# Kernel optimization log

Measured on AMD Instinct MI355X. Metric: run time of the kernel, lower is better.

## Reference

```python
import jax, jax.numpy as jnp
import numpy as np

N, E, IN_DIM, C = 30000, 300000, 128, 16


def _xavier(key, shape):
    fan_in, fan_out = shape[1], shape[0]
    lim = np.sqrt(6.0 / (fan_in + fan_out))
    return jax.random.uniform(key, shape, jnp.float32, -lim, lim)


def layernorm(x, g, b, eps=1e-5):
    mu = jnp.mean(x, axis=-1, keepdims=True)
    var = jnp.var(x, axis=-1, keepdims=True)
    return (x - mu) * jax.lax.rsqrt(var + eps) * g + b


def setup_inputs() -> dict:
    key = jax.random.key(0)
    ks = jax.random.split(key, 8)
    D9 = C * 9            # 144
    DI = C * (C * 2)      # 512
    return {
        "x": jax.random.normal(ks[0], (N, IN_DIM), jnp.float32),
        "h": jax.random.normal(ks[1], (N, IN_DIM), jnp.float32),
        "local_frames": jax.random.normal(ks[2], (N, 3, 3), jnp.float32),
        "edge_index": jax.random.randint(ks[3], (2, E), 0, N, jnp.int64),
        "batch": jnp.zeros((N,), jnp.int64),
        # tensor_init: Linear(IN_DIM,144) LN SiLU Linear(144,144) LN SiLU
        "W1": _xavier(ks[4], (D9, IN_DIM)), "b1": jnp.zeros((D9,), jnp.float32),
        "g1": jnp.ones((D9,), jnp.float32), "be1": jnp.zeros((D9,), jnp.float32),
        "W2": _xavier(ks[5], (D9, D9)), "b2": jnp.zeros((D9,), jnp.float32),
        "g2": jnp.ones((D9,), jnp.float32), "be2": jnp.zeros((D9,), jnp.float32),
        # tensor_interaction: Linear(2*IN_DIM,512) LN Sigmoid
        "Wi": _xavier(ks[6], (DI, 2 * IN_DIM)), "bi": jnp.zeros((DI,), jnp.float32),
        "gi": jnp.ones((DI,), jnp.float32), "bei": jnp.zeros((DI,), jnp.float32),
    }


def reference(x, h, local_frames, edge_index, batch,
              W1, b1, g1, be1, W2, b2, g2, be2, Wi, bi, gi, bei):
    n = x.shape[0]
    row, col = edge_index[0], edge_index[1]

    # tensor_init(h) -> [N, C, 3, 3]
    t = jax.nn.silu(layernorm(h @ W1.T + b1, g1, be1))
    t = jax.nn.silu(layernorm(t @ W2.T + b2, g2, be2))
    tensors = t.reshape(n, C, 3, 3)

    hi, hj = h[col], h[row]
    ti, tj = tensors[col], tensors[row]
    Ri, Rj = local_frames[col], local_frames[row]

    # R_rel = Ri^T @ Rj : [E,3,3]
    R_rel = jnp.einsum('eki,ekj->eij', Ri, Rj)
    # rotate sender tensor: R_rel T R_rel^T
    tj_in_i = jnp.einsum('eik,eckl,elj->ecij', R_rel, tj, R_rel)

    stacked_tensor = jnp.concatenate([ti, tj_in_i], axis=1)          # [E,2C,3,3]
    stacked_scalars = jnp.concatenate([hi, hj], axis=-1)             # [E,2*IN_DIM]
    w = jax.nn.sigmoid(layernorm(stacked_scalars @ Wi.T + bi, gi, bei))
    int_weights = w.reshape(-1, 2 * C, C)                            # [E,2C,C]

    t_new = jnp.einsum('ekij,ekc->ecij', stacked_tensor, int_weights)  # [E,C,3,3]

    t_out = jax.ops.segment_sum(t_new, col, num_segments=n)           # [N,C,3,3]
    t_out = 0.5 * (t_out + jnp.swapaxes(t_out, -1, -2))
    return t_out
```

## Files before the change

kernel.cpp:

```cpp
#include <hip/hip_runtime.h>

#define NN 30000
#define EE 300000
#define HD 128
#define D9 144
#define ECHUNK 150000

typedef unsigned int uint32;
typedef unsigned short u16;
typedef __attribute__((ext_vector_type(8))) short short8;
typedef __attribute__((ext_vector_type(4))) float f32x4;
typedef __attribute__((ext_vector_type(4))) uint32 u32x4;

__device__ __forceinline__ float sigmoidf_(float x){ return 1.0f/(1.0f+__expf(-x)); }
__device__ __forceinline__ float siluf_(float x){ return x/(1.0f+__expf(-x)); }
__device__ __forceinline__ u16 f2bf(float f){
  uint32 u = __float_as_uint(f);
  return (u16)((u + 0x7fffu + ((u>>16)&1u)) >> 16);
}
__device__ __forceinline__ float bf2f(u16 b){ return __uint_as_float(((uint32)b)<<16); }
__device__ __forceinline__ float bflo(uint32 u){ return __uint_as_float(u<<16); }
__device__ __forceinline__ float bfhi(uint32 u){ return __uint_as_float(u & 0xffff0000u); }
__device__ __forceinline__ uint32 pk2(float a, float b){ return (uint32)f2bf(a) | ((uint32)f2bf(b)<<16); }

__global__ __launch_bounds__(256) void cvt_wq_k(const float* __restrict__ Wi, u16* __restrict__ Wq){
  int i = blockIdx.x*256 + threadIdx.x;
  if (i < 512*128){
    int n = i >> 7, k = i & 127;
    float xl = Wi[n*256 + k];
    float xr = Wi[n*256 + 128 + k];
    u16 lh = f2bf(xl);
    Wq[i]          = lh;
    Wq[65536 + i]  = f2bf(xl - bf2f(lh));
    u16 rh = f2bf(xr);
    Wq[131072 + i] = rh;
    Wq[196608 + i] = f2bf(xr - bf2f(rh));
  }
}

__global__ __launch_bounds__(256) void cvt_w1s_k(const float* __restrict__ W1, u16* __restrict__ W1s){
  int i = blockIdx.x*256 + threadIdx.x;
  if (i < 144*128){
    float x = W1[i];
    u16 hh = f2bf(x);
    W1s[i] = hh;
    W1s[18432 + i] = f2bf(x - bf2f(hh));
  }
}
__global__ __launch_bounds__(256) void cvt_w2s_k(const float* __restrict__ W2, u16* __restrict__ W2s){
  int i = blockIdx.x*256 + threadIdx.x;
  if (i < 144*160){
    int r = i / 160, k = i - r*160;
    float x = (k < 144) ? W2[r*144 + k] : 0.f;
    u16 hh = f2bf(x);
    W2s[i] = hh;
    W2s[23040 + i] = f2bf(x - bf2f(hh));
  }
}
__global__ __launch_bounds__(256) void cvt_gt_k(const float* __restrict__ gi, const float* __restrict__ bei,
                                                float* __restrict__ gt, float* __restrict__ bet){
  int i = blockIdx.x*256 + threadIdx.x;
  if (i < 512){
    int c = i & 15, k = i >> 4;
    gt [c*32 + k] = gi[i];
    bet[c*32 + k] = bei[i];
  }
}

__global__ __launch_bounds__(256) void hist_k(const int* __restrict__ ei, uint32* __restrict__ start){
  int e = blockIdx.x*256 + threadIdx.x;
  if (e < EE){
    int col = ei[EE + e];
    col = col < 0 ? 0 : (col >= NN ? NN-1 : col);
    atomicAdd(&start[col], 1u);
  }
}

__global__ __launch_bounds__(1024) void scan_k(uint32* __restrict__ start){
  __shared__ uint32 part[1024];
  const int t = threadIdx.x;
  const int base = t * 30;
  uint32 loc[30];
  uint32 s = 0;
  #pragma unroll
  for (int i = 0; i < 30; ++i){
    int idx = base + i;
    uint32 cv = (idx < NN) ? start[idx] : 0u;
    loc[i] = s;
    s += cv;
  }
  part[t] = s;
  __syncthreads();
  for (int off = 1; off < 1024; off <<= 1){
    uint32 add = (t >= off) ? part[t - off] : 0u;
    __syncthreads();
    part[t] += add;
    __syncthreads();
  }
  uint32 pre = (t == 0) ? 0u : part[t - 1];
  #pragma unroll
  for (int i = 0; i < 30; ++i){
    int idx = base + i;
    if (idx < NN) start[idx] = pre + loc[i];
  }
}

__global__ __launch_bounds__(256) void scatter_k(const int* __restrict__ ei,
                                                 uint32* __restrict__ start,
                                                 u16* __restrict__ srow, u16* __restrict__ scol){
  int e = blockIdx.x*256 + threadIdx.x;
  if (e < EE){
    int row = ei[e];
    row = row < 0 ? 0 : (row >= NN ? NN-1 : row);
    int col = ei[EE + e];
    col = col < 0 ? 0 : (col >= NN ? NN-1 : col);
    uint32 pos = atomicAdd(&start[col], 1u);
    srow[pos] = (u16)row;
    scol[pos] = (u16)col;
  }
}

__global__ __launch_bounds__(256) void tensor_init2_k(
    const float* __restrict__ h,
    const u16* __restrict__ W1s, const u16* __restrict__ W2s,
    const float* __restrict__ b1, const float* __restrict__ g1, const float* __restrict__ be1,
    const float* __restrict__ b2, const float* __restrict__ g2, const float* __restrict__ be2,
    float* __restrict__ tens_t)
{
  __shared__ float t1s[16 * 164];
  __shared__ float pool[160];

  const int t = threadIdx.x;
  const int w = t >> 6, l = t & 63, lr = l & 15, lg = l >> 4;
  const int nb = blockIdx.x * 16;
  const int ntile = (w == 0) ? 3 : 2;
  int tiles[3]; tiles[0] = 2*w; tiles[1] = 2*w + 1; tiles[2] = 8;

  f32x4 acc[3];
  #pragma unroll
  for (int ti = 0; ti < 3; ++ti) acc[ti] = (f32x4){0,0,0,0};
  {
    const float* qA = h + (size_t)(nb + lr) * HD + lg*8;
    #pragma unroll
    for (int ks = 0; ks < 4; ++ks){
      float4 x0 = *(const float4*)(qA + ks*32);
      float4 x1 = *(const float4*)(qA + ks*32 + 4);
      float xs[8] = {x0.x, x0.y, x0.z, x0.w, x1.x, x1.y, x1.z, x1.w};
      short8 aH, aL;
      #pragma unroll
      for (int j = 0; j < 8; ++j){
        u16 hh = f2bf(xs[j]);
        aH[j] = (short)hh;
        aL[j] = (short)f2bf(xs[j] - bf2f(hh));
      }
      for (int ti = 0; ti < ntile; ++ti){
        const u16* b = W1s + (tiles[ti]*16 + lr)*128 + lg*8 + ks*32;
        short8 bH = *(const short8*)b;
        short8 bL = *(const short8*)(b + 18432);
        acc[ti] = __builtin_amdgcn_mfma_f32_16x16x32_bf16(aH, bH, acc[ti], 0, 0, 0);
        acc[ti] = __builtin_amdgcn_mfma_f32_16x16x32_bf16(aL, bH, acc[ti], 0, 0, 0);
        acc[ti] = __builtin_amdgcn_mfma_f32_16x16x32_bf16(aH, bL, acc[ti], 0, 0, 0);
      }
    }
  }
  for (int ti = 0; ti < ntile; ++ti){
    float bb = b1[tiles[ti]*16 + lr];
    #pragma unroll
    for (int r = 0; r < 4; ++r) acc[ti][r] += bb;
  }
  {
    float ps[4], pq[4];
    #pragma unroll
    for (int r = 0; r < 4; ++r){
      float s = 0.f, q = 0.f;
      for (int ti = 0; ti < ntile; ++ti){ s += acc[ti][r]; q += acc[ti][r]*acc[ti][r]; }
      ps[r] = s; pq[r] = q;
    }
    #pragma unroll
    for (int off = 1; off < 16; off <<= 1)
      #pragma unroll
      for (int r = 0; r < 4; ++r){ ps[r] += __shfl_xor(ps[r], off); pq[r] += __shfl_xor(pq[r], off); }
    if (lr == 0){
      #pragma unroll
      for (int r = 0; r < 4; ++r){
        pool[w*32 + (lg*4 + r)*2 + 0] = ps[r];
        pool[w*32 + (lg*4 + r)*2 + 1] = pq[r];
      }
    }
  }
  __syncthreads();
  if (t < 16){
    float s = pool[t*2] + pool[32 + t*2] + pool[64 + t*2] + pool[96 + t*2];
    float q = pool[t*2+1] + pool[32 + t*2+1] + pool[64 + t*2+1] + pool[96 + t*2+1];
    float mu = s * (1.0f/144.0f);
    pool[128 + t] = mu;
    pool[144 + t] = rsqrtf(q * (1.0f/144.0f) - mu*mu + 1e-5f);
  }
  __syncthreads();
  for (int ti = 0; ti < ntile; ++ti){
    int col = tiles[ti]*16 + lr;
    float gg = g1[col], bb = be1[col];
    #pragma unroll
    for (int r = 0; r < 4; ++r){
      int node = lg*4 + r;
      float mu = pool[128 + node], rs = pool[144 + node];
      t1s[node*164 + col] = siluf_((acc[ti][r] - mu) * rs * gg + bb);
    }
  }
  t1s[(t >> 4)*164 + 144 + (t & 15)] = 0.f;
  __syncthreads();

  #pragma unroll
  for (int ti = 0; ti < 3; ++ti) acc[ti] = (f32x4){0,0,0,0};
  #pragma unroll
  for (int ks = 0; ks < 5; ++ks){
    float4 x0 = *(const float4*)&t1s[lr*164 + lg*8 + ks*32];
    float4 x1 = *(const float4*)&t1s[lr*164 + lg*8 + ks*32 + 4];
    float xs[8] = {x0.x, x0.y, x0.z, x0.w, x1.x, x1.y, x1.z, x1.w};
    short8 aH, aL;
    #pragma unroll
    for (int j = 0; j < 8; ++j){
      u16 hh = f2bf(xs[j]);
      aH[j] = (short)hh;
      aL[j] = (short)f2bf(xs[j] - bf2f(hh));
    }
    for (int ti = 0; ti < ntile; ++ti){
      const u16* b = W2s + (tiles[ti]*16 + lr)*160 + lg*8 + ks*32;
      short8 bH = *(const short8*)b;
      short8 bL = *(const short8*)(b + 23040);
      acc[ti] = __builtin_amdgcn_mfma_f32_16x16x32_bf16(aH, bH, acc[ti], 0, 0, 0);
      acc[ti] = __builtin_amdgcn_mfma_f32_16x16x32_bf16(aL, bH, acc[ti], 0, 0, 0);
      acc[ti] = __builtin_amdgcn_mfma_f32_16x16x32_bf16(aH, bL, acc[ti], 0, 0, 0);
    }
  }
  for (int ti = 0; ti < ntile; ++ti){
    float bb = b2[tiles[ti]*16 + lr];
    #pragma unroll
    for (int r = 0; r < 4; ++r) acc[ti][r] += bb;
  }
  __syncthreads();
  {
    float ps[4], pq[4];
    #pragma unroll
    for (int r = 0; r < 4; ++r){
      float s = 0.f, q = 0.f;
      for (int ti = 0; ti < ntile; ++ti){ s += acc[ti][r]; q += acc[ti][r]*acc[ti][r]; }
      ps[r] = s; pq[r] = q;
    }
    #pragma unroll
    for (int off = 1; off < 16; off <<= 1)
      #pragma unroll
      for (int r = 0; r < 4; ++r){ ps[r] += __shfl_xor(ps[r], off); pq[r] += __shfl_xor(pq[r], off); }
    if (lr == 0){
      #pragma unroll
      for (int r = 0; r < 4; ++r){
        pool[w*32 + (lg*4 + r)*2 + 0] = ps[r];
        pool[w*32 + (lg*4 + r)*2 + 1] = pq[r];
      }
    }
  }
  __syncthreads();
  if (t < 16){
    float s = pool[t*2] + pool[32 + t*2] + pool[64 + t*2] + pool[96 + t*2];
    float q = pool[t*2+1] + pool[32 + t*2+1] + pool[64 + t*2+1] + pool[96 + t*2+1];
    float mu = s * (1.0f/144.0f);
    pool[128 + t] = mu;
    pool[144 + t] = rsqrtf(q * (1.0f/144.0f) - mu*mu + 1e-5f);
  }
  __syncthreads();
  for (int ti = 0; ti < ntile; ++ti){
    int col = tiles[ti]*16 + lr;
    float gg = g2[col], bb = be2[col];
    int c = col / 9, m = col - c*9;
    #pragma unroll
    for (int r = 0; r < 4; ++r){
      int node = lg*4 + r;
      float mu = pool[128 + node], rs = pool[144 + node];
      float val = siluf_((acc[ti][r] - mu) * rs * gg + bb);
      tens_t[(size_t)(nb + node)*144 + m*16 + c] = val;
    }
  }
}

__global__ __launch_bounds__(256) void node_gemm_k(
    const float* __restrict__ h, const u16* __restrict__ Wq,
    const float* __restrict__ bi,
    u16* __restrict__ uu_t, u16* __restrict__ v16_t)
{
  const int t = threadIdx.x;
  const int w = t >> 6, l = t & 63, lr = l & 15, lg = l >> 4;
  const int nb = blockIdx.x * 16;

  const float* qA = h + (size_t)(nb + lr) * HD + lg*8;
  f32x4 au[8], av[8];
  #pragma unroll
  for (int nt = 0; nt < 8; ++nt){ au[nt] = (f32x4){0,0,0,0}; av[nt] = (f32x4){0,0,0,0}; }

  #pragma unroll
  for (int ks = 0; ks < 4; ++ks){
    float4 x0 = *(const float4*)(qA + ks*32);
    float4 x1 = *(const float4*)(qA + ks*32 + 4);
    float xs[8] = {x0.x, x0.y, x0.z, x0.w, x1.x, x1.y, x1.z, x1.w};
    short8 aH, aL;
    #pragma unroll
    for (int j = 0; j < 8; ++j){
      u16 hh = f2bf(xs[j]);
      aH[j] = (short)hh;
      aL[j] = (short)f2bf(xs[j] - bf2f(hh));
    }
    #pragma unroll
    for (int nt = 0; nt < 8; ++nt){
      const u16* bu = Wq + (w*128 + nt*16 + lr)*128 + lg*8 + ks*32;
      short8 bH = *(const short8*)bu;
      short8 bL = *(const short8*)(bu + 65536);
      au[nt] = __builtin_amdgcn_mfma_f32_16x16x32_bf16(aH, bH, au[nt], 0, 0, 0);
      au[nt] = __builtin_amdgcn_mfma_f32_16x16x32_bf16(aL, bH, au[nt], 0, 0, 0);
      au[nt] = __builtin_amdgcn_mfma_f32_16x16x32_bf16(aH, bL, au[nt], 0, 0, 0);
      const u16* bv = bu + 131072;
      short8 cH = *(const short8*)bv;
      short8 cL = *(const short8*)(bv + 65536);
      av[nt] = __builtin_amdgcn_mfma_f32_16x16x32_bf16(aH, cH, av[nt], 0, 0, 0);
      av[nt] = __builtin_amdgcn_mfma_f32_16x16x32_bf16(aL, cH, av[nt], 0, 0, 0);
      av[nt] = __builtin_amdgcn_mfma_f32_16x16x32_bf16(aH, cL, av[nt], 0, 0, 0);
    }
  }

  float bb[8];
  #pragma unroll
  for (int nt = 0; nt < 8; ++nt) bb[nt] = bi[w*128 + nt*16 + lr];

  #pragma unroll
  for (int r = 0; r < 4; ++r){
    size_t node = nb + lg*4 + r;
    u32x4 pu;
    pu.x = pk2(au[0][r]+bb[0], au[1][r]+bb[1]);
    pu.y = pk2(au[2][r]+bb[2], au[3][r]+bb[3]);
    pu.z = pk2(au[4][r]+bb[4], au[5][r]+bb[5]);
    pu.w = pk2(au[6][r]+bb[6], au[7][r]+bb[7]);
    *(u32x4*)(uu_t + node*512 + lr*32 + w*8) = pu;
    u32x4 pv;
    pv.x = pk2(av[0][r], av[1][r]); pv.y = pk2(av[2][r], av[3][r]);
    pv.z = pk2(av[4][r], av[5][r]); pv.w = pk2(av[6][r], av[7][r]);
    *(u32x4*)(v16_t + node*512 + lr*32 + w*8) = pv;
  }
}

__global__ __launch_bounds__(256) void edge_par_k(
    const u16* __restrict__ uu_t, const u16* __restrict__ v16_t,
    const float* __restrict__ frames, const float* __restrict__ tens_t,
    const float* __restrict__ gt, const float* __restrict__ bet,
    const u16* __restrict__ srow, const u16* __restrict__ scol,
    int ebase, float* __restrict__ tn)
{
  const int t = threadIdx.x;
  const int le = t >> 4, c = t & 15;
  const int eloc = blockIdx.x*16 + le;
  const size_t idx = (size_t)ebase + eloc;
  const int row = (int)srow[idx], col = (int)scol[idx];

  float z[32];
  {
    const u16* up = uu_t + (size_t)col*512 + c*32;
    const u16* vp = v16_t + (size_t)row*512 + c*32;
    #pragma unroll
    for (int q = 0; q < 4; ++q){
      u32x4 ua = *(const u32x4*)(up + q*8);
      u32x4 va = *(const u32x4*)(vp + q*8);
      z[q*8+0] = bflo(ua.x)+bflo(va.x); z[q*8+1] = bfhi(ua.x)+bfhi(va.x);
      z[q*8+2] = bflo(ua.y)+bflo(va.y); z[q*8+3] = bfhi(ua.y)+bfhi(va.y);
      z[q*8+4] = bflo(ua.z)+bflo(va.z); z[q*8+5] = bfhi(ua.z)+bfhi(va.z);
      z[q*8+6] = bflo(ua.w)+bflo(va.w); z[q*8+7] = bfhi(ua.w)+bfhi(va.w);
    }
  }

  float s = 0.f, q2 = 0.f;
  #pragma unroll
  for (int k = 0; k < 32; ++k){ s += z[k]; q2 += z[k]*z[k]; }
  #pragma unroll
  for (int off = 1; off < 16; off <<= 1){ s += __shfl_xor(s, off); q2 += __shfl_xor(q2, off); }
  float mu = s * (1.0f/512.0f);
  float rs = rsqrtf(q2 * (1.0f/512.0f) - mu*mu + 1e-5f);

  {
    const float* gp = gt  + c*32;
    const float* bp = bet + c*32;
    #pragma unroll
    for (int kq = 0; kq < 8; ++kq){
      float4 g4 = *(const float4*)(gp + kq*4);
      float4 b4 = *(const float4*)(bp + kq*4);
      z[kq*4+0] = sigmoidf_((z[kq*4+0]-mu)*rs*g4.x + b4.x);
      z[kq*4+1] = sigmoidf_((z[kq*4+1]-mu)*rs*g4.y + b4.y);
      z[kq*4+2] = sigmoidf_((z[kq*4+2]-mu)*rs*g4.z + b4.z);
      z[kq*4+3] = sigmoidf_((z[kq*4+3]-mu)*rs*g4.w + b4.w);
    }
  }

  float o[9], G[9];
  {
    const float* ti = tens_t + (size_t)col*144;
    const float* tj = tens_t + (size_t)row*144;
    #pragma unroll
    for (int m = 0; m < 9; ++m){
      float a = 0.f, g = 0.f;
      #pragma unroll
      for (int kq = 0; kq < 4; ++kq){
        float4 t4 = *(const float4*)(ti + m*16 + kq*4);
        a += t4.x*z[kq*4+0] + t4.y*z[kq*4+1] + t4.z*z[kq*4+2] + t4.w*z[kq*4+3];
        float4 u4 = *(const float4*)(tj + m*16 + kq*4);
        g += u4.x*z[16+kq*4+0] + u4.y*z[16+kq*4+1] + u4.z*z[16+kq*4+2] + u4.w*z[16+kq*4+3];
      }
      o[m] = a; G[m] = g;
    }
  }

  {
    const float* Ri = frames + (size_t)col*9;
    const float* Rj = frames + (size_t)row*9;
    float R[9];
    #pragma unroll
    for (int i = 0; i < 3; ++i)
      #pragma unroll
      for (int j = 0; j < 3; ++j)
        R[i*3+j] = Ri[i]*Rj[j] + Ri[3+i]*Rj[3+j] + Ri[6+i]*Rj[6+j];
    float A[9];
    #pragma unroll
    for (int i = 0; i < 3; ++i)
      #pragma unroll
      for (int j = 0; j < 3; ++j)
        A[i*3+j] = R[i*3+0]*G[0+j] + R[i*3+1]*G[3+j] + R[i*3+2]*G[6+j];
    #pragma unroll
    for (int i = 0; i < 3; ++i)
      #pragma unroll
      for (int j = 0; j < 3; ++j)
        o[i*3+j] += A[i*3+0]*R[0+j] + A[i*3+1]*R[3+j] + A[i*3+2]*R[6+j];
  }

  float s01 = 0.5f*(o[1]+o[3]), s02 = 0.5f*(o[2]+o[6]), s12 = 0.5f*(o[5]+o[7]);
  float* tp = tn + (size_t)eloc*96 + c*6;
  float2 w0 = {o[0], s01}, w1 = {s02, o[4]}, w2 = {s12, o[8]};
  *(float2*)tp = w0;
  *(float2*)(tp+2) = w1;
  *(float2*)(tp+4) = w2;
}

__global__ __launch_bounds__(256) void segsum_k(
    const float* __restrict__ tn, const uint32* __restrict__ start,
    uint32 ebase, uint32 eend, int first, float* __restrict__ out)
{
  int tid = blockIdx.x*256 + threadIdx.x;
  if (tid >= NN*16) return;
  int n = tid >> 4, c = tid & 15;
  uint32 beg = (n == 0) ? 0u : start[n-1];
  uint32 end = start[n];
  uint32 b = beg > ebase ? beg : ebase;
  uint32 e = end < eend ? end : eend;

  float* op = out + (size_t)n*144 + c*9;
  float a0, a1, a2, a3, a4, a5;
  if (first){ a0=a1=a2=a3=a4=a5=0.f; }
  else { a0=op[0]; a1=op[1]; a2=op[2]; a3=op[4]; a4=op[5]; a5=op[8]; }

  for (uint32 i = b; i < e; ++i){
    const float* tp = tn + (size_t)(i - ebase)*96 + c*6;
    float2 x0 = *(const float2*)tp;
    float2 x1 = *(const float2*)(tp+2);
    float2 x2 = *(const float2*)(tp+4);
    a0 += x0.x; a1 += x0.y; a2 += x1.x; a3 += x1.y; a4 += x2.x; a5 += x2.y;
  }

  op[0] = a0; op[1] = a1; op[2] = a2;
  op[3] = a1; op[4] = a3; op[5] = a4;
  op[6] = a2; op[7] = a4; op[8] = a5;
}

extern "C" void kernel_launch(void* const* d_in, const int* in_sizes, int n_in,
                              void* d_out, int out_size, void* d_ws, size_t ws_size,
                              hipStream_t stream) {
    const float* h      = (const float*)d_in[1];
    const float* frames = (const float*)d_in[2];
    const int*   ei     = (const int*)d_in[3];
    const float* W1  = (const float*)d_in[5];
    const float* b1  = (const float*)d_in[6];
    const float* g1  = (const float*)d_in[7];
    const float* be1 = (const float*)d_in[8];
    const float* W2  = (const float*)d_in[9];
    const float* b2  = (const float*)d_in[10];
    const float* g2  = (const float*)d_in[11];
    const float* be2 = (const float*)d_in[12];
    const float* Wi  = (const float*)d_in[13];
    const float* bi  = (const float*)d_in[14];
    const float* gi  = (const float*)d_in[15];
    const float* bei = (const float*)d_in[16];

    float* out = (float*)d_out;

    u16*    uu_t  = (u16*)d_ws;
    u16*    v16_t = (u16*)  ((char*)d_ws + 30720000);
    float*  tens_t= (float*)((char*)d_ws + 61440000);
    u16*    Wq    = (u16*)  ((char*)d_ws + 78720000);
    u16*    W1s   = (u16*)  ((char*)d_ws + 79244288);
    u16*    W2s   = (u16*)  ((char*)d_ws + 79318016);
    float*  gt    = (float*)((char*)d_ws + 79410176);
    float*  bet   = (float*)((char*)d_ws + 79412224);
    uint32* start = (uint32*)((char*)d_ws + 79414272);
    u16*    srow  = (u16*)  ((char*)d_ws + 79534272);
    u16*    scol  = (u16*)  ((char*)d_ws + 80134272);
    float*  tn    = (float*)((char*)d_ws + 80734272);

    hipMemsetAsync(start, 0, NN * sizeof(uint32), stream);

    cvt_wq_k<<<256, 256, 0, stream>>>(Wi, Wq);
    cvt_w1s_k<<<72, 256, 0, stream>>>(W1, W1s);
    cvt_w2s_k<<<90, 256, 0, stream>>>(W2, W2s);
    cvt_gt_k<<<2, 256, 0, stream>>>(gi, bei, gt, bet);
    tensor_init2_k<<<NN/16, 256, 0, stream>>>(h, W1s, W2s, b1, g1, be1, b2, g2, be2, tens_t);
    node_gemm_k<<<NN/16, 256, 0, stream>>>(h, Wq, bi, uu_t, v16_t);
    hist_k<<<(EE + 255)/256, 256, 0, stream>>>(ei, start);
    scan_k<<<1, 1024, 0, stream>>>(start);
    scatter_k<<<(EE + 255)/256, 256, 0, stream>>>(ei, start, srow, scol);

    edge_par_k<<<ECHUNK/16, 256, 0, stream>>>(uu_t, v16_t, frames, tens_t, gt, bet, srow, scol, 0, tn);
    segsum_k<<<(NN*16 + 255)/256, 256, 0, stream>>>(tn, start, 0u, (uint32)ECHUNK, 1, out);
    edge_par_k<<<ECHUNK/16, 256, 0, stream>>>(uu_t, v16_t, frames, tens_t, gt, bet, srow, scol, ECHUNK, tn);
    segsum_k<<<(NN*16 + 255)/256, 256, 0, stream>>>(tn, start, (uint32)ECHUNK, (uint32)EE, 0, out);
}
```

Before: 652.9 us.

## Fuse node kernels, merge weight conversions, store edge outputs as bf16 in one pass

Merges the four weight-conversion kernels into one launch and fuses the interaction-weight node GEMM into the tensor-init kernel, so h is loaded and split into bf16 hi/lo parts only once. Per-edge outputs are now packed as bf16 pairs, halving the intermediate buffer. This lets all edges be processed in a single edge-kernel launch plus one segment-sum instead of two chunks. The cost is reduced precision in the per-edge partial sums before accumulation, and higher register pressure in the fused node kernel, which may lower occupancy.

```diff
diff --git a/kernel.cpp b/kernel.cpp
--- a/kernel.cpp
+++ b/kernel.cpp
@@ -4,7 +4,6 @@
 #define EE 300000
 #define HD 128
 #define D9 144
-#define ECHUNK 150000
 
 typedef unsigned int uint32;
 typedef unsigned short u16;
@@ -23,7 +22,13 @@
 __device__ __forceinline__ float bfhi(uint32 u){ return __uint_as_float(u & 0xffff0000u); }
 __device__ __forceinline__ uint32 pk2(float a, float b){ return (uint32)f2bf(a) | ((uint32)f2bf(b)<<16); }
 
-__global__ __launch_bounds__(256) void cvt_wq_k(const float* __restrict__ Wi, u16* __restrict__ Wq){
+__global__ __launch_bounds__(256) void cvt_all_k(
+    const float* __restrict__ Wi, u16* __restrict__ Wq,
+    const float* __restrict__ W1, u16* __restrict__ W1s,
+    const float* __restrict__ W2, u16* __restrict__ W2s,
+    const float* __restrict__ gi, const float* __restrict__ bei,
+    float* __restrict__ gt, float* __restrict__ bet)
+{
   int i = blockIdx.x*256 + threadIdx.x;
   if (i < 512*128){
     int n = i >> 7, k = i & 127;
@@ -36,19 +41,12 @@
     Wq[131072 + i] = rh;
     Wq[196608 + i] = f2bf(xr - bf2f(rh));
   }
-}
-
-__global__ __launch_bounds__(256) void cvt_w1s_k(const float* __restrict__ W1, u16* __restrict__ W1s){
-  int i = blockIdx.x*256 + threadIdx.x;
   if (i < 144*128){
     float x = W1[i];
     u16 hh = f2bf(x);
     W1s[i] = hh;
     W1s[18432 + i] = f2bf(x - bf2f(hh));
   }
-}
-__global__ __launch_bounds__(256) void cvt_w2s_k(const float* __restrict__ W2, u16* __restrict__ W2s){
-  int i = blockIdx.x*256 + threadIdx.x;
   if (i < 144*160){
     int r = i / 160, k = i - r*160;
     float x = (k < 144) ? W2[r*144 + k] : 0.f;
@@ -56,10 +54,6 @@
     W2s[i] = hh;
     W2s[23040 + i] = f2bf(x - bf2f(hh));
   }
-}
-__global__ __launch_bounds__(256) void cvt_gt_k(const float* __restrict__ gi, const float* __restrict__ bei,
-                                                float* __restrict__ gt, float* __restrict__ bet){
-  int i = blockIdx.x*256 + threadIdx.x;
   if (i < 512){
     int c = i & 15, k = i >> 4;
     gt [c*32 + k] = gi[i];
@@ -120,12 +114,13 @@
   }
 }
 
-__global__ __launch_bounds__(256) void tensor_init2_k(
-    const float* __restrict__ h,
+__global__ __launch_bounds__(256) void node_all_k(
+    const float* __restrict__ h, const u16* __restrict__ Wq,
+    const float* __restrict__ bi,
     const u16* __restrict__ W1s, const u16* __restrict__ W2s,
     const float* __restrict__ b1, const float* __restrict__ g1, const float* __restrict__ be1,
     const float* __restrict__ b2, const float* __restrict__ g2, const float* __restrict__ be2,
-    float* __restrict__ tens_t)
+    u16* __restrict__ uu_t, u16* __restrict__ v16_t, float* __restrict__ tens_t)
 {
   __shared__ float t1s[16 * 164];
   __shared__ float pool[160];
@@ -136,9 +131,7 @@
   const int ntile = (w == 0) ? 3 : 2;
   int tiles[3]; tiles[0] = 2*w; tiles[1] = 2*w + 1; tiles[2] = 8;
 
-  f32x4 acc[3];
-  #pragma unroll
-  for (int ti = 0; ti < 3; ++ti) acc[ti] = (f32x4){0,0,0,0};
+  short8 aH[4], aL[4];
   {
     const float* qA = h + (size_t)(nb + lr) * HD + lg*8;
     #pragma unroll
@@ -146,21 +139,68 @@
       float4 x0 = *(const float4*)(qA + ks*32);
       float4 x1 = *(const float4*)(qA + ks*32 + 4);
       float xs[8] = {x0.x, x0.y, x0.z, x0.w, x1.x, x1.y, x1.z, x1.w};
-      short8 aH, aL;
       #pragma unroll
       for (int j = 0; j < 8; ++j){
         u16 hh = f2bf(xs[j]);
-        aH[j] = (short)hh;
-        aL[j] = (short)f2bf(xs[j] - bf2f(hh));
+        aH[ks][j] = (short)hh;
+        aL[ks][j] = (short)f2bf(xs[j] - bf2f(hh));
       }
-      for (int ti = 0; ti < ntile; ++ti){
-        const u16* b = W1s + (tiles[ti]*16 + lr)*128 + lg*8 + ks*32;
-        short8 bH = *(const short8*)b;
-        short8 bL = *(const short8*)(b + 18432);
-        acc[ti] = __builtin_amdgcn_mfma_f32_16x16x32_bf16(aH, bH, acc[ti], 0, 0, 0);
-        acc[ti] = __builtin_amdgcn_mfma_f32_16x16x32_bf16(aL, bH, acc[ti], 0, 0, 0);
-        acc[ti] = __builtin_amdgcn_mfma_f32_16x16x32_bf16(aH, bL, acc[ti], 0, 0, 0);
+    }
+  }
+
+  {
+    f32x4 au[8], av[8];
+    #pragma unroll
+    for (int nt = 0; nt < 8; ++nt){ au[nt] = (f32x4){0,0,0,0}; av[nt] = (f32x4){0,0,0,0}; }
+    #pragma unroll
+    for (int ks = 0; ks < 4; ++ks){
+      #pragma unroll
+      for (int nt = 0; nt < 8; ++nt){
+        const u16* bu = Wq + (w*128 + nt*16 + lr)*128 + lg*8 + ks*32;
+        short8 bH = *(const short8*)bu;
+        short8 bL = *(const short8*)(bu + 65536);
+        au[nt] = __builtin_amdgcn_mfma_f32_16x16x32_bf16(aH[ks], bH, au[nt], 0, 0, 0);
+        au[nt] = __builtin_amdgcn_mfma_f32_16x16x32_bf16(aL[ks], bH, au[nt], 0, 0, 0);
+        au[nt] = __builtin_amdgcn_mfma_f32_16x16x32_bf16(aH[ks], bL, au[nt], 0, 0, 0);
+        const u16* bv = bu + 131072;
+        short8 cH = *(const short8*)bv;
+        short8 cL = *(const short8*)(bv + 65536);
+        av[nt] = __builtin_amdgcn_mfma_f32_16x16x32_bf16(aH[ks], cH, av[nt], 0, 0, 0);
+        av[nt] = __builtin_amdgcn_mfma_f32_16x16x32_bf16(aL[ks], cH, av[nt], 0, 0, 0);
+        av[nt] = __builtin_amdgcn_mfma_f32_16x16x32_bf16(aH[ks], cL, av[nt], 0, 0, 0);
       }
+    }
+    float bb[8];
+    #pragma unroll
+    for (int nt = 0; nt < 8; ++nt) bb[nt] = bi[w*128 + nt*16 + lr];
+    #pragma unroll
+    for (int r = 0; r < 4; ++r){
+      size_t node = nb + lg*4 + r;
+      u32x4 pu;
+      pu.x = pk2(au[0][r]+bb[0], au[1][r]+bb[1]);
+      pu.y = pk2(au[2][r]+bb[2], au[3][r]+bb[3]);
+      pu.z = pk2(au[4][r]+bb[4], au[5][r]+bb[5]);
+      pu.w = pk2(au[6][r]+bb[6], au[7][r]+bb[7]);
+      *(u32x4*)(uu_t + node*512 + lr*32 + w*8) = pu;
+      u32x4 pv;
+      pv.x = pk2(av[0][r], av[1][r]); pv.y = pk2(av[2][r], av[3][r]);
+      pv.z = pk2(av[4][r], av[5][r]); pv.w = pk2(av[6][r], av[7][r]);
+      *(u32x4*)(v16_t + node*512 + lr*32 + w*8) = pv;
+    }
+  }
+
+  f32x4 acc[3];
+  #pragma unroll
+  for (int ti = 0; ti < 3; ++ti) acc[ti] = (f32x4){0,0,0,0};
+  #pragma unroll
+  for (int ks = 0; ks < 4; ++ks){
+    for (int ti = 0; ti < ntile; ++ti){
+      const u16* b = W1s + (tiles[ti]*16 + lr)*128 + lg*8 + ks*32;
+      short8 bH = *(const short8*)b;
+      short8 bL = *(const short8*)(b + 18432);
+      acc[ti] = __builtin_amdgcn_mfma_f32_16x16x32_bf16(aH[ks], bH, acc[ti], 0, 0, 0);
+      acc[ti] = __builtin_amdgcn_mfma_f32_16x16x32_bf16(aL[ks], bH, acc[ti], 0, 0, 0);
+      acc[ti] = __builtin_amdgcn_mfma_f32_16x16x32_bf16(aH[ks], bL, acc[ti], 0, 0, 0);
     }
   }
   for (int ti = 0; ti < ntile; ++ti){
@@ -217,20 +257,20 @@
     float4 x0 = *(const float4*)&t1s[lr*164 + lg*8 + ks*32];
     float4 x1 = *(const float4*)&t1s[lr*164 + lg*8 + ks*32 + 4];
     float xs[8] = {x0.x, x0.y, x0.z, x0.w, x1.x, x1.y, x1.z, x1.w};
-    short8 aH, aL;
+    short8 a2H, a2L;
     #pragma unroll
     for (int j = 0; j < 8; ++j){
       u16 hh = f2bf(xs[j]);
-      aH[j] = (short)hh;
-      aL[j] = (short)f2bf(xs[j] - bf2f(hh));
+      a2H[j] = (short)hh;
+      a2L[j] = (short)f2bf(xs[j] - bf2f(hh));
     }
     for (int ti = 0; ti < ntile; ++ti){
       const u16* b = W2s + (tiles[ti]*16 + lr)*160 + lg*8 + ks*32;
       short8 bH = *(const short8*)b;
       short8 bL = *(const short8*)(b + 23040);
-      acc[ti] = __builtin_amdgcn_mfma_f32_16x16x32_bf16(aH, bH, acc[ti], 0, 0, 0);
-      acc[ti] = __builtin_amdgcn_mfma_f32_16x16x32_bf16(aL, bH, acc[ti], 0, 0, 0);
-      acc[ti] = __builtin_amdgcn_mfma_f32_16x16x32_bf16(aH, bL, acc[ti], 0, 0, 0);
+      acc[ti] = __builtin_amdgcn_mfma_f32_16x16x32_bf16(a2H, bH, acc[ti], 0, 0, 0);
+      acc[ti] = __builtin_amdgcn_mfma_f32_16x16x32_bf16(a2L, bH, acc[ti], 0, 0, 0);
+      acc[ti] = __builtin_amdgcn_mfma_f32_16x16x32_bf16(a2H, bL, acc[ti], 0, 0, 0);
     }
   }
   for (int ti = 0; ti < ntile; ++ti){
@@ -282,81 +322,17 @@
   }
 }
 
-__global__ __launch_bounds__(256) void node_gemm_k(
-    const float* __restrict__ h, const u16* __restrict__ Wq,
-    const float* __restrict__ bi,
-    u16* __restrict__ uu_t, u16* __restrict__ v16_t)
-{
-  const int t = threadIdx.x;
-  const int w = t >> 6, l = t & 63, lr = l & 15, lg = l >> 4;
-  const int nb = blockIdx.x * 16;
-
-  const float* qA = h + (size_t)(nb + lr) * HD + lg*8;
-  f32x4 au[8], av[8];
-  #pragma unroll
-  for (int nt = 0; nt < 8; ++nt){ au[nt] = (f32x4){0,0,0,0}; av[nt] = (f32x4){0,0,0,0}; }
-
-  #pragma unroll
-  for (int ks = 0; ks < 4; ++ks){
-    float4 x0 = *(const float4*)(qA + ks*32);
-    float4 x1 = *(const float4*)(qA + ks*32 + 4);
-    float xs[8] = {x0.x, x0.y, x0.z, x0.w, x1.x, x1.y, x1.z, x1.w};
-    short8 aH, aL;
-    #pragma unroll
-    for (int j = 0; j < 8; ++j){
-      u16 hh = f2bf(xs[j]);
-      aH[j] = (short)hh;
-      aL[j] = (short)f2bf(xs[j] - bf2f(hh));
-    }
-    #pragma unroll
-    for (int nt = 0; nt < 8; ++nt){
-      const u16* bu = Wq + (w*128 + nt*16 + lr)*128 + lg*8 + ks*32;
-      short8 bH = *(const short8*)bu;
-      short8 bL = *(const short8*)(bu + 65536);
-      au[nt] = __builtin_amdgcn_mfma_f32_16x16x32_bf16(aH, bH, au[nt], 0, 0, 0);
-      au[nt] = __builtin_amdgcn_mfma_f32_16x16x32_bf16(aL, bH, au[nt], 0, 0, 0);
-      au[nt] = __builtin_amdgcn_mfma_f32_16x16x32_bf16(aH, bL, au[nt], 0, 0, 0);
-      const u16* bv = bu + 131072;
-      short8 cH = *(const short8*)bv;
-      short8 cL = *(const short8*)(bv + 65536);
-      av[nt] = __builtin_amdgcn_mfma_f32_16x16x32_bf16(aH, cH, av[nt], 0, 0, 0);
-      av[nt] = __builtin_amdgcn_mfma_f32_16x16x32_bf16(aL, cH, av[nt], 0, 0, 0);
-      av[nt] = __builtin_amdgcn_mfma_f32_16x16x32_bf16(aH, cL, av[nt], 0, 0, 0);
-    }
-  }
-
-  float bb[8];
-  #pragma unroll
-  for (int nt = 0; nt < 8; ++nt) bb[nt] = bi[w*128 + nt*16 + lr];
-
-  #pragma unroll
-  for (int r = 0; r < 4; ++r){
-    size_t node = nb + lg*4 + r;
-    u32x4 pu;
-    pu.x = pk2(au[0][r]+bb[0], au[1][r]+bb[1]);
-    pu.y = pk2(au[2][r]+bb[2], au[3][r]+bb[3]);
-    pu.z = pk2(au[4][r]+bb[4], au[5][r]+bb[5]);
-    pu.w = pk2(au[6][r]+bb[6], au[7][r]+bb[7]);
-    *(u32x4*)(uu_t + node*512 + lr*32 + w*8) = pu;
-    u32x4 pv;
-    pv.x = pk2(av[0][r], av[1][r]); pv.y = pk2(av[2][r], av[3][r]);
-    pv.z = pk2(av[4][r], av[5][r]); pv.w = pk2(av[6][r], av[7][r]);
-    *(u32x4*)(v16_t + node*512 + lr*32 + w*8) = pv;
-  }
-}
-
 __global__ __launch_bounds__(256) void edge_par_k(
     const u16* __restrict__ uu_t, const u16* __restrict__ v16_t,
     const float* __restrict__ frames, const float* __restrict__ tens_t,
     const float* __restrict__ gt, const float* __restrict__ bet,
     const u16* __restrict__ srow, const u16* __restrict__ scol,
-    int ebase, float* __restrict__ tn)
+    uint32* __restrict__ tn)
 {
   const int t = threadIdx.x;
   const int le = t >> 4, c = t & 15;
-  const int eloc = blockIdx.x*16 + le;
-  const size_t idx = (size_t)ebase + eloc;
-  const int row = (int)srow[idx], col = (int)scol[idx];
+  const int e = blockIdx.x*16 + le;
+  const int row = (int)srow[e], col = (int)scol[e];
 
   float z[32];
   {
@@ -436,38 +412,32 @@
   }
 
   float s01 = 0.5f*(o[1]+o[3]), s02 = 0.5f*(o[2]+o[6]), s12 = 0.5f*(o[5]+o[7]);
-  float* tp = tn + (size_t)eloc*96 + c*6;
-  float2 w0 = {o[0], s01}, w1 = {s02, o[4]}, w2 = {s12, o[8]};
-  *(float2*)tp = w0;
-  *(float2*)(tp+2) = w1;
-  *(float2*)(tp+4) = w2;
+  uint32* tp = tn + (size_t)e*48 + c*3;
+  tp[0] = pk2(o[0], s01);
+  tp[1] = pk2(s02, o[4]);
+  tp[2] = pk2(s12, o[8]);
 }
 
 __global__ __launch_bounds__(256) void segsum_k(
-    const float* __restrict__ tn, const uint32* __restrict__ start,
-    uint32 ebase, uint32 eend, int first, float* __restrict__ out)
+    const uint32* __restrict__ tn, const uint32* __restrict__ start,
+    float* __restrict__ out)
 {
   int tid = blockIdx.x*256 + threadIdx.x;
   if (tid >= NN*16) return;
   int n = tid >> 4, c = tid & 15;
   uint32 beg = (n == 0) ? 0u : start[n-1];
   uint32 end = start[n];
-  uint32 b = beg > ebase ? beg : ebase;
-  uint32 e = end < eend ? end : eend;
+
+  float a0=0.f, a1=0.f, a2=0.f, a3=0.f, a4=0.f, a5=0.f;
+  for (uint32 i = beg; i < end; ++i){
+    const uint32* tp = tn + (size_t)i*48 + c*3;
+    uint32 x0 = tp[0], x1 = tp[1], x2 = tp[2];
+    a0 += bflo(x0); a1 += bfhi(x0);
+    a2 += bflo(x1); a3 += bfhi(x1);
+    a4 += bflo(x2); a5 += bfhi(x2);
+  }
 
   float* op = out + (size_t)n*144 + c*9;
-  float a0, a1, a2, a3, a4, a5;
-  if (first){ a0=a1=a2=a3=a4=a5=0.f; }
-  else { a0=op[0]; a1=op[1]; a2=op[2]; a3=op[4]; a4=op[5]; a5=op[8]; }
-
-  for (uint32 i = b; i < e; ++i){
-    const float* tp = tn + (size_t)(i - ebase)*96 + c*6;
-    float2 x0 = *(const float2*)tp;
-    float2 x1 = *(const float2*)(tp+2);
-    float2 x2 = *(const float2*)(tp+4);
-    a0 += x0.x; a1 += x0.y; a2 += x1.x; a3 += x1.y; a4 += x2.x; a5 += x2.y;
-  }
-
   op[0] = a0; op[1] = a1; op[2] = a2;
   op[3] = a1; op[4] = a3; op[5] = a4;
   op[6] = a2; op[7] = a4; op[8] = a5;
@@ -505,22 +475,16 @@
     uint32* start = (uint32*)((char*)d_ws + 79414272);
     u16*    srow  = (u16*)  ((char*)d_ws + 79534272);
     u16*    scol  = (u16*)  ((char*)d_ws + 80134272);
-    float*  tn    = (float*)((char*)d_ws + 80734272);
+    uint32* tn    = (uint32*)((char*)d_ws + 80734272);
 
     hipMemsetAsync(start, 0, NN * sizeof(uint32), stream);
 
-    cvt_wq_k<<<256, 256, 0, stream>>>(Wi, Wq);
-    cvt_w1s_k<<<72, 256, 0, stream>>>(W1, W1s);
-    cvt_w2s_k<<<90, 256, 0, stream>>>(W2, W2s);
-    cvt_gt_k<<<2, 256, 0, stream>>>(gi, bei, gt, bet);
-    tensor_init2_k<<<NN/16, 256, 0, stream>>>(h, W1s, W2s, b1, g1, be1, b2, g2, be2, tens_t);
-    node_gemm_k<<<NN/16, 256, 0, stream>>>(h, Wq, bi, uu_t, v16_t);
+    cvt_all_k<<<256, 256, 0, stream>>>(Wi, Wq, W1, W1s, W2, W2s, gi, bei, gt, bet);
+    node_all_k<<<NN/16, 256, 0, stream>>>(h, Wq, bi, W1s, W2s, b1, g1, be1, b2, g2, be2,
+                                          uu_t, v16_t, tens_t);
     hist_k<<<(EE + 255)/256, 256, 0, stream>>>(ei, start);
     scan_k<<<1, 1024, 0, stream>>>(start);
     scatter_k<<<(EE + 255)/256, 256, 0, stream>>>(ei, start, srow, scol);
-
-    edge_par_k<<<ECHUNK/16, 256, 0, stream>>>(uu_t, v16_t, frames, tens_t, gt, bet, srow, scol, 0, tn);
-    segsum_k<<<(NN*16 + 255)/256, 256, 0, stream>>>(tn, start, 0u, (uint32)ECHUNK, 1, out);
-    edge_par_k<<<ECHUNK/16, 256, 0, stream>>>(uu_t, v16_t, frames, tens_t, gt, bet, srow, scol, ECHUNK, tn);
-    segsum_k<<<(NN*16 + 255)/256, 256, 0, stream>>>(tn, start, (uint32)ECHUNK, (uint32)EE, 0, out);
-}
+    edge_par_k<<<EE/16, 256, 0, stream>>>(uu_t, v16_t, frames, tens_t, gt, bet, srow, scol, tn);
+    segsum_k<<<(NN*16 + 255)/256, 256, 0, stream>>>(tn, start, out);
+}
```

Result: faster. 610.3 us (-6.5%).
